# Performance work log

Hardware: AMD Instinct MI355X
Metric: run time of the kernel (lower is better)

## Reference

```python
import jax, jax.numpy as jnp
import numpy as np

N, K, C, R, S = 10000, 16, 32, 32, 64
D = 9  # per-channel irrep dim of interaction feats: 0e(1)+1o(3)+2e(5)
AVG_NEIGH = 16.0
EPS = 1e-6

_rng = np.random.default_rng(0)
# fixed constant coupling tensors (deterministic stand-ins for CG coefficients; structure matches e3nn paths)
CG112 = jnp.asarray(_rng.standard_normal((3, 3, 5)) * 0.2, jnp.float32)  # 1o x 1o -> 2e
CG121 = jnp.asarray(_rng.standard_normal((3, 5, 3)) * 0.2, jnp.float32)  # 1o x 2e -> 1o
# symmetric tensor-product bases U[order, ir_out]: shape (D,)*order + (mul, ir_dim)
MULS = {3: {'0e': 3, '1o': 2}, 2: {'0e': 2, '1o': 1}, 1: {'0e': 1, '1o': 1}}
IRDIM = {'0e': 1, '1o': 3}
U = {(o, ir): jnp.asarray(_rng.standard_normal((D,) * o + (MULS[o][ir], IRDIM[ir])) * (0.3 ** o), jnp.float32)
     for o in (3, 2, 1) for ir in ('0e', '1o')}


def _normnorm(arrs):
    # E3NormNorm: per-node RMS normalization over channel/component axes
    return [a / jnp.sqrt(jnp.mean(a * a, axis=tuple(range(1, a.ndim)), keepdims=True) + EPS) for a in arrs]


def _sph_harm(vec):
    # real spherical harmonics l=1,2 (component normalization) on normalized vectors
    r = vec / (jnp.linalg.norm(vec, axis=-1, keepdims=True) + EPS)
    x, y, z = r[..., 0], r[..., 1], r[..., 2]
    sh1 = jnp.sqrt(3.0) * r
    c = jnp.sqrt(15.0)
    sh2 = jnp.stack([c * x * y, c * y * z, jnp.sqrt(5.0) / 2 * (3 * z * z - 1), c * x * z, c / 2 * (x * x - y * y)], axis=-1)
    return sh1, sh2


def _forward(node_s, node_v, vectors, radial_embedding, species_table, Wu0, Wu1, radW, radb, ln_g, ln_b,
             Wd0, Wd1, Wd2, w3_0e, w3_1o, w2_0e, w2_1o, w1_0e, w1_1o, P0, P1, Wskip0, Wskip1, Wread,
             receivers, node_specie):
    n, c = node_s.shape
    inv = 1.0 / jnp.sqrt(1.0 * c)
    # ---- InteractionBlock: linear_up + norm ----
    s = node_s @ Wu0 * inv
    v = jnp.einsum('nci,cd->ndi', node_v, Wu1) * inv
    s, v = _normnorm([s, v])
    # ---- MessagePassingConvolution: sender = node i broadcast over its K=16 neighbors ----
    sh1, sh2 = _sph_harm(vectors)  # [n,K,3], [n,K,5]
    m0a = jnp.broadcast_to(s[:, None, :], (n, K, c))                       # prefix 0e
    m0b = jnp.einsum('nci,nki->nkc', v, sh1) / jnp.sqrt(3.0)               # 1o x 1o -> 0e
    m1a = jnp.broadcast_to(v[:, None], (n, K, c, 3))                       # prefix 1o
    m1b = jnp.einsum('nc,nki->nkci', s, sh1) / jnp.sqrt(3.0)               # 0e x 1o -> 1o
    m1c = jnp.einsum('nci,nkp,ipj->nkcj', v, sh2, CG121)                   # 1o x 2e -> 1o
    m2a = jnp.einsum('nc,nkp->nkcp', s, sh2) / jnp.sqrt(5.0)               # 0e x 2e -> 2e
    m2b = jnp.einsum('nci,nkj,ijp->nkcp', v, sh1, CG112)                   # 1o x 1o -> 2e
    M0 = jnp.concatenate([m0a, m0b], axis=-1)      # [n,K,2C]
    M1 = jnp.concatenate([m1a, m1b, m1c], axis=2)  # [n,K,3C,3]
    M2 = jnp.concatenate([m2a, m2b], axis=2)       # [n,K,2C,5]
    # radial mix: linear + layernorm, one weight per irrep (7C total)
    rad = radial_embedding @ radW + radb
    mu = rad.mean(-1, keepdims=True)
    var = rad.var(-1, keepdims=True)
    rad = ln_g * (rad - mu) / jnp.sqrt(var + EPS) + ln_b
    r0, r1, r2 = rad[..., :2 * c], rad[..., 2 * c:5 * c], rad[..., 5 * c:]
    M0 = M0 * r0
    M1 = M1 * r1[..., None]
    M2 = M2 * r2[..., None]
    # scatter-add messages to receivers, normalize by sqrt(avg_num_neighbors)
    idx = receivers.reshape(-1)
    sc = 1.0 / jnp.sqrt(AVG_NEIGH)
    o0 = jnp.zeros((n, 2 * c), M0.dtype).at[idx].add(M0.reshape(n * K, 2 * c)) * sc
    o1 = jnp.zeros((n, 3 * c, 3), M1.dtype).at[idx].add(M1.reshape(n * K, 3 * c, 3)) * sc
    o2 = jnp.zeros((n, 2 * c, 5), M2.dtype).at[idx].add(M2.reshape(n * K, 2 * c, 5)) * sc
    o0, o1, o2 = _normnorm([o0, o1, o2])
    # linear_down to interaction_irreps Cx(0e+1o+2e), then norm
    A0 = o0 @ Wd0 / jnp.sqrt(2.0 * c)
    A1 = jnp.einsum('nmi,md->ndi', o1, Wd1) / jnp.sqrt(3.0 * c)
    A2 = jnp.einsum('nmi,md->ndi', o2, Wd2) / jnp.sqrt(2.0 * c)
    A0, A1, A2 = _normnorm([A0, A1, A2])
    # ---- EquivariantProductBasisBlock: species-gathered symmetric contraction ----
    x_sym = jnp.concatenate([A0[:, :, None], A1, A2], axis=-1)  # [n, C, D=9]
    species_ind = species_table[node_specie]                    # [n, R]
    Wsym = {(3, '0e'): w3_0e, (3, '1o'): w3_1o, (2, '0e'): w2_0e, (2, '1o'): w2_1o, (1, '0e'): w1_0e, (1, '1o'): w1_1o}
    out = {}
    for order in (3, 2, 1):
        for ir in ('0e', '1o'):
            u = U[(order, ir)]
            w = jnp.einsum('be,ekc->bkc', species_ind, Wsym[(order, ir)])
            if ir not in out:
                out[ir] = ('new', jnp.einsum('...jki,bkc,bcj->bc...i', u, w, x_sym))
            else:
                out[ir] = out[ir] + jnp.einsum('...ki,bkc->bc...i', u, w)
        for ir in ('0e', '1o'):
            if isinstance(out[ir], tuple):
                out[ir] = out[ir][1]  # creation order already consumed one x
            else:
                out[ir] = jnp.einsum('bc...ji,bcj->bc...i', out[ir], x_sym)
    sym_s = out['0e'][..., 0]  # [n, C]
    sym_v = out['1o']          # [n, C, 3]
    # proj_out linear
    ps = sym_s @ P0 * inv
    pv = jnp.einsum('nci,cd->ndi', sym_v, P1) * inv
    # species-indexed skip connection
    skip_s = jnp.einsum('nc,ncd->nd', node_s, Wskip0[node_specie]) * inv
    skip_v = jnp.einsum('nci,ncd->ndi', node_v, Wskip1[node_specie]) * inv
    s_out = ps + skip_s
    v_out = pv + skip_v
    # linear readout (output_irreps = 1x0e)
    read = s_out @ Wread * inv
    return jnp.concatenate([s_out, v_out.reshape(n, 3 * c), read], axis=-1)


def setup_inputs():
    ks = jax.random.split(jax.random.key(0), 32)
    f = lambda i, shape: jax.random.normal(ks[i], shape, jnp.float32)
    return {
        'node_s': f(0, (N, C)),
        'node_v': f(1, (N, C, 3)),
        'vectors': f(2, (N, K, 3)),
        'radial_embedding': f(3, (N, K, R)),
        'receivers': jax.random.randint(ks[4], (N, K), 0, N),
        'node_specie': jax.random.randint(ks[5], (N,), 0, S),
        'species_table': f(6, (S, R)),
        'Wu0': f(7, (C, C)), 'Wu1': f(8, (C, C)),
        'radW': f(9, (R, 7 * C)), 'radb': jnp.zeros((7 * C,), jnp.float32),
        'ln_g': jnp.ones((7 * C,), jnp.float32), 'ln_b': jnp.zeros((7 * C,), jnp.float32),
        'Wd0': f(11, (2 * C, C)), 'Wd1': f(12, (3 * C, C)), 'Wd2': f(13, (2 * C, C)),
        'w3_0e': f(14, (R, 3, C)), 'w3_1o': f(15, (R, 2, C)),
        'w2_0e': f(16, (R, 2, C)), 'w2_1o': f(17, (R, 1, C)),
        'w1_0e': f(18, (R, 1, C)), 'w1_1o': f(19, (R, 1, C)),
        'P0': f(20, (C, C)), 'P1': f(21, (C, C)),
        'Wskip0': f(22, (S, C, C)), 'Wskip1': f(23, (S, C, C)),
        'Wread': f(24, (C, 1)),
    }


def reference(node_s, node_v, vectors, radial_embedding, receivers, node_specie, species_table, Wu0, Wu1,
              radW, radb, ln_g, ln_b, Wd0, Wd1, Wd2, w3_0e, w3_1o, w2_0e, w2_1o, w1_0e, w1_1o,
              P0, P1, Wskip0, Wskip1, Wread):
    return _forward(node_s, node_v, vectors, radial_embedding, species_table, Wu0, Wu1, radW, radb, ln_g, ln_b,
                    Wd0, Wd1, Wd2, w3_0e, w3_1o, w2_0e, w2_1o, w1_0e, w1_1o, P0, P1, Wskip0, Wskip1, Wread,
                    receivers, node_specie)
```

## Files before the change

### kernel.cpp

```cpp
#include <hip/hip_runtime.h>
#include <cmath>
#include <stdint.h>

typedef unsigned long long u64;
typedef unsigned __int128 u128;

#define EPSF 1e-6f

#define OFF_RAW 0L
#define OFF_S   7168L
#define OFF_G   8960L
#define GSP_SZ  28032L
#define OFF_SN  (OFF_G + 64L*GSP_SZ)
#define OFF_VN  (OFF_SN + 320000L)
#define FLOAT_END (OFF_VN + 960000L)
#define OFF_RAD (FLOAT_END + 262144L)
#define RAD_REQ_BYTES ((size_t)(OFF_RAD + 35840000L) * 4)

#define IOFF_DEG   0
#define IOFF_OFFS  10000
#define IOFF_CUR   20001
#define IOFF_EL    30001
#define IOFF_SCNT  190001
#define IOFF_SOFF  190065
#define IOFF_SCUR  190130
#define IOFF_NORD  190194
#define IOFF_TRI   200194
#define IOFF_PAIR  200359


__device__ __forceinline__ u128 pcg_mul128() {
  return ((u128)2549297995355413924ULL << 64) | (u128)4865540595714422341ULL;
}
struct Pcg {
  u128 state, inc;
  __device__ __forceinline__ u64 next() {
    state = state * pcg_mul128() + inc;
    u64 hi = (u64)(state >> 64), lo = (u64)state;
    unsigned rot = (unsigned)(hi >> 58);
    u64 x = hi ^ lo;
    return (x >> rot) | (x << ((64u - rot) & 63u));
  }
};
__device__ __forceinline__ double u64_to_dbl(u64 u) {
  return (double)(u >> 11) * (1.0 / 9007199254740992.0);
}
__device__ __forceinline__ unsigned ss_hashmix(unsigned v, unsigned &hc) {
  v ^= hc; hc *= 0x931e8875u; v *= hc; v ^= v >> 16; return v;
}
__device__ __forceinline__ unsigned ss_mix(unsigned x, unsigned y) {
  unsigned r = 0xca01f9ddu * x - 0x4973f715u * y; r ^= r >> 16; return r;
}

#define NBUF 8192
#define NBM  8191
#define PERTH 32
#define NDRAW 7092
#define NSEG  222

__global__ __launch_bounds__(256) void k_constants(float* __restrict__ wsf, int* __restrict__ wsi)
{
  __shared__ double wi[256], fi[256];
  __shared__ u64 ki[256];
  __shared__ u64 buf[NBUF];
  __shared__ float zv[NBUF];
  __shared__ unsigned char cons[NBUF];
  __shared__ unsigned short jmp[NBUF];
  __shared__ unsigned short heads[NSEG];
  __shared__ u64 sseed[4];
  __shared__ u64 stst[512], enst[512];
  __shared__ double scl[8];
  __shared__ int flag;
  const int tid = threadIdx.x;
  float* raw = wsf + OFF_RAW;

  if (tid == 0) {
    flag = 0;
    unsigned hc = 0x43b0d7e5u;
    unsigned pool[4];
    for (int i = 0; i < 4; i++) pool[i] = ss_hashmix(0u, hc);
    for (int s = 0; s < 4; s++)
      for (int d = 0; d < 4; d++)
        if (s != d) pool[d] = ss_mix(pool[d], ss_hashmix(pool[s], hc));
    unsigned hb = 0x8b51f9ddu;
    u64 sw[4];
    {
      unsigned w8[8];
      for (int i = 0; i < 8; i++) {
        unsigned dv = pool[i & 3];
        dv ^= hb; hb *= 0x58f38dedu; dv *= hb; dv ^= dv >> 16;
        w8[i] = dv;
      }
      for (int k2 = 0; k2 < 4; k2++) sw[k2] = (u64)w8[2*k2] | ((u64)w8[2*k2+1] << 32);
    }
    u128 initstate = ((u128)sw[0] << 64) | (u128)sw[1];
    u128 initseq   = ((u128)sw[2] << 64) | (u128)sw[3];
    u128 inc_ = (initseq << 1) | (u128)1;
    u128 S0 = inc_;
    S0 += initstate;
    S0 = S0 * pcg_mul128() + inc_;
    sseed[0] = (u64)(S0 >> 64);   sseed[1] = (u64)S0;
    sseed[2] = (u64)(inc_ >> 64); sseed[3] = (u64)inc_;
    double p2 = pow(0.3, 2.0), p3 = pow(0.3, 3.0);
    scl[0]=0.2; scl[1]=0.2; scl[2]=p3; scl[3]=p3; scl[4]=p2; scl[5]=p2; scl[6]=0.3; scl[7]=0.3;
    const double m1 = 4503599627370496.0;
    const double ZR = 3.6541528853610087963519472518;
    double dn = ZR, tn = ZR;
    const double vn = 4.92867323399e-3;
    double fv = exp(-0.5 * dn * dn);
    double q = vn / fv;
    ki[0] = (u64)((dn / q) * m1);
    ki[1] = 0;
    wi[0] = q / m1;  wi[255] = dn / m1;
    fi[0] = 1.0;     fi[255] = fv;
    for (int i = 254; i >= 1; i--) {
      dn = sqrt(-2.0 * log(vn / dn + fv));
      ki[i+1] = (u64)((dn / tn) * m1);
      tn = dn;
      fv = exp(-0.5 * dn * dn);
      fi[i] = fv;
      wi[i] = dn / m1;
    }
    int mcnt = 0;
    for (int a = 0; a < 9; a++)
      for (int b = a; b < 9; b++)
        for (int j3 = b; j3 < 9; j3++)
          wsi[IOFF_TRI + (mcnt++)] = a | (b << 4) | (j3 << 8);
    int pcnt = 0;
    for (int a = 0; a < 9; a++)
      for (int b = a; b < 9; b++)
        wsi[IOFF_PAIR + (pcnt++)] = a | (b << 4);
  }
  __syncthreads();

  {
    u128 S0   = ((u128)sseed[0] << 64) | (u128)sseed[1];
    u128 inc_ = ((u128)sseed[2] << 64) | (u128)sseed[3];
    u128 aR = (u128)1, cR = (u128)0;
    u128 aP = pcg_mul128(), cP = inc_;
    unsigned e = (unsigned)tid * PERTH;
    while (e) {
      if (e & 1u) { cR = aP * cR + cP; aR = aP * aR; }
      cP = aP * cP + cP;
      aP = aP * aP;
      e >>= 1;
    }
    Pcg g; g.inc = inc_; g.state = aR * S0 + cR;
    stst[tid*2] = (u64)(g.state >> 64); stst[tid*2+1] = (u64)g.state;
    #pragma unroll 4
    for (int k = 0; k < PERTH; k++) buf[tid*PERTH + k] = g.next();
    enst[tid*2] = (u64)(g.state >> 64); enst[tid*2+1] = (u64)g.state;
  }
  __syncthreads();
  if (tid < 255) {
    if (stst[(tid+1)*2] != enst[tid*2] || stst[(tid+1)*2+1] != enst[tid*2+1])
      atomicOr(&flag, 1);
  }
  if (tid == 0) {
    if (fabs(u64_to_dbl(buf[0]) - 0.6369616873214543) > 1e-12) atomicOr(&flag, 1);
  }
  __syncthreads();
  if (flag && tid == 0) {
    u128 S0   = ((u128)sseed[0] << 64) | (u128)sseed[1];
    u128 inc_ = ((u128)sseed[2] << 64) | (u128)sseed[3];
    Pcg g; g.state = S0; g.inc = inc_;
    for (int k = 0; k < NBUF; k++) buf[k] = g.next();
  }
  __syncthreads();

  const double ZRd  = 3.6541528853610087963519472518;
  const double ZIRd = 0.27366123732975827203338247596;
  for (int k = 0; k < PERTH; k++) {
    const int p = tid*PERTH + k;
    int pos = p;
    int consumed = 0;
    double z = 0.0;
    u64 r = buf[pos & NBM]; pos++; consumed++;
    for (int guard = 0; guard < 64; guard++) {
      int idx = (int)(r & 0xff);
      r >>= 8;
      int sgn = (int)(r & 1);
      u64 rabs = (r >> 1) & 0x000fffffffffffffULL;
      double x = (double)rabs * wi[idx];
      if (sgn) x = -x;
      if (rabs < ki[idx]) { z = x; break; }
      if (idx == 0) {
        double xx = 0.0, yy = 0.0;
        for (int g2 = 0; g2 < 64; g2++) {
          u64 ua = buf[pos & NBM]; pos++; consumed++;
          u64 ub = buf[pos & NBM]; pos++; consumed++;
          xx = -ZIRd * log1p(-u64_to_dbl(ua));
          yy = -log1p(-u64_to_dbl(ub));
          if (yy + yy > xx * xx) break;
        }
        z = ((rabs >> 8) & 1) ? -(ZRd + xx) : (ZRd + xx);
        break;
      } else {
        u64 u = buf[pos & NBM]; pos++; consumed++;
        if ((fi[idx-1] - fi[idx]) * u64_to_dbl(u) + fi[idx] < exp(-0.5 * x * x)) { z = x; break; }
      }
      r = buf[pos & NBM]; pos++; consumed++;
    }
    zv[p] = (float)z;
    cons[p] = (unsigned char)(consumed > 255 ? 255 : consumed);
  }
  __syncthreads();

  {
    int pos[PERTH];
    #pragma unroll
    for (int k = 0; k < PERTH; k++) pos[k] = tid*PERTH + k;
    for (int s = 0; s < 32; s++) {
      #pragma unroll
      for (int k = 0; k < PERTH; k++) {
        int np = pos[k] + (int)cons[pos[k]];
        pos[k] = (np > NBM) ? NBM : np;
      }
    }
    #pragma unroll
    for (int k = 0; k < PERTH; k++) jmp[tid*PERTH + k] = (unsigned short)pos[k];
  }
  __syncthreads();

  if (tid == 0) {
    int pos = 0;
    for (int m = 0; m < NSEG; m++) { heads[m] = (unsigned short)pos; pos = (int)jmp[pos]; }
  }
  __syncthreads();

  if (tid < NSEG) {
    int pos = (int)heads[tid];
    const int i0 = tid * 32;
    for (int k = 0; k < 32; k++) {
      const int i = i0 + k;
      if (i >= NDRAW) break;
      double sc;
      if      (i < 90)   sc = scl[0];
      else if (i < 6651) sc = scl[2];
      else if (i < 7056) sc = scl[4];
      else               sc = scl[6];
      raw[i] = (float)((double)zv[pos] * sc);
      int np = pos + (int)cons[pos];
      pos = (np > NBM) ? NBM : np;
    }
  }
}

__global__ __launch_bounds__(256) void k_stables(float* __restrict__ wsf, const int* __restrict__ wsi)
{
  const int tid = threadIdx.x;
  const float* raw = wsf + OFF_RAW;
  float* Sb = wsf + OFF_S;
  for (int idx = tid; idx < 495; idx += 256) {
    int m = idx / 3, k2 = idx % 3;
    int tp = wsi[IOFF_TRI + m];
    int a = tp & 15, b = (tp >> 4) & 15, j3 = (tp >> 8) & 15;
    int P[6][3] = {{a,b,j3},{a,j3,b},{b,a,j3},{b,j3,a},{j3,a,b},{j3,b,a}};
    float s = 0.f;
    for (int t = 0; t < 6; t++) {
      bool dup = false;
      for (int u = 0; u < t; u++)
        if (P[u][0]==P[t][0] && P[u][1]==P[t][1] && P[u][2]==P[t][2]) { dup = true; break; }
      if (!dup) s += raw[90 + ((P[t][0]*9 + P[t][1])*9 + P[t][2])*3 + k2];
    }
    Sb[m*3 + k2] = s;
  }
  for (int idx = tid; idx < 990; idx += 256) {
    int m = idx / 6, r6 = idx % 6, k2 = r6 / 3, i = r6 % 3;
    int tp = wsi[IOFF_TRI + m];
    int a = tp & 15, b = (tp >> 4) & 15, j3 = (tp >> 8) & 15;
    int P[6][3] = {{a,b,j3},{a,j3,b},{b,a,j3},{b,j3,a},{j3,a,b},{j3,b,a}};
    float s = 0.f;
    for (int t = 0; t < 6; t++) {
      bool dup = false;
      for (int u = 0; u < t; u++)
        if (P[u][0]==P[t][0] && P[u][1]==P[t][1] && P[u][2]==P[t][2]) { dup = true; break; }
      if (!dup) s += raw[2277 + (((P[t][0]*9 + P[t][1])*9 + P[t][2])*2 + k2)*3 + i];
    }
    Sb[495 + (m*2 + k2)*3 + i] = s;
  }
  for (int idx = tid; idx < 90; idx += 256) {
    int m = idx / 2, k2 = idx % 2;
    int pp = wsi[IOFF_PAIR + m]; int a = pp & 15, b = (pp >> 4) & 15;
    float s = raw[6651 + (a*9 + b)*2 + k2];
    if (a != b) s += raw[6651 + (b*9 + a)*2 + k2];
    Sb[1485 + idx] = s;
  }
  for (int idx = tid; idx < 135; idx += 256) {
    int m = idx / 3, i = idx % 3;
    int pp = wsi[IOFF_PAIR + m]; int a = pp & 15, b = (pp >> 4) & 15;
    float s = raw[6813 + (a*9 + b)*3 + i];
    if (a != b) s += raw[6813 + (b*9 + a)*3 + i];
    Sb[1575 + idx] = s;
  }
  for (int idx = tid; idx < 9;  idx += 256) Sb[1710 + idx] = raw[7056 + idx];
  for (int idx = tid; idx < 27; idx += 256) Sb[1719 + idx] = raw[7065 + idx];
}

__global__ __launch_bounds__(256) void k_gtable(
    const float* __restrict__ stab,
    const float* __restrict__ w30e, const float* __restrict__ w31o,
    const float* __restrict__ w20e, const float* __restrict__ w21o,
    const float* __restrict__ w10e, const float* __restrict__ w11o,
    float* __restrict__ wsf)
{
  const int sp = blockIdx.x, tid = threadIdx.x;
  float* Gsp = wsf + OFF_G + (long)sp * GSP_SZ;
  __shared__ float st[32];
  if (tid < 32) st[tid] = stab[sp*32 + tid];
  __syncthreads();
  for (int t = tid; t < 320; t += 256) {
    const float* W; int kc, kcs;
    if (t < 96)       { W = w30e; kc = t;       kcs = 96; }
    else if (t < 160) { W = w31o; kc = t - 96;  kcs = 64; }
    else if (t < 224) { W = w20e; kc = t - 160; kcs = 64; }
    else if (t < 256) { W = w21o; kc = t - 224; kcs = 32; }
    else if (t < 288) { W = w10e; kc = t - 256; kcs = 32; }
    else              { W = w11o; kc = t - 288; kcs = 32; }
    float a = 0.f;
    for (int e = 0; e < 32; e++) a += st[e] * W[e*kcs + kc];
    Gsp[t] = a;
  }
}

__global__ __launch_bounds__(256) void k_nodeupd(
    const float* __restrict__ ns, const float* __restrict__ nv,
    const float* __restrict__ Wu0, const float* __restrict__ Wu1,
    float* __restrict__ wsf)
{
  const int tid = threadIdx.x;
  const int nn = blockIdx.x * 8 + (tid >> 5);
  const int c = tid & 31;
  const float INV = 0.17677669529663687f;
  float s = 0.f;
  for (int e = 0; e < 32; e++) s += ns[nn*32 + e] * Wu0[e*32 + c];
  s *= INV;
  float v0 = 0, v1 = 0, v2 = 0;
  for (int e = 0; e < 32; e++) {
    const float w = Wu1[e*32 + c];
    const float* p = nv + (long)(nn*32 + e)*3;
    v0 += p[0]*w; v1 += p[1]*w; v2 += p[2]*w;
  }
  v0 *= INV; v1 *= INV; v2 *= INV;
  float ss = s*s;
  for (int m = 16; m >= 1; m >>= 1) ss += __shfl_xor(ss, m);
  float sv = v0*v0 + v1*v1 + v2*v2;
  for (int m = 16; m >= 1; m >>= 1) sv += __shfl_xor(sv, m);
  float rs = rsqrtf(ss * (1.f/32.f) + EPSF);
  float rv = rsqrtf(sv * (1.f/96.f) + EPSF);
  wsf[OFF_SN + nn*32 + c] = s * rs;
  float* vp = wsf + OFF_VN + (long)(nn*32 + c)*3;
  vp[0] = v0*rv; vp[1] = v1*rv; vp[2] = v2*rv;
}

#define RB_E 32
__global__ __launch_bounds__(256) void k_radial(
    const float* __restrict__ remb, const float* __restrict__ radW,
    const float* __restrict__ radb, const float* __restrict__ ln_g,
    const float* __restrict__ ln_b, float* __restrict__ wsf)
{
  __shared__ float er[RB_E][33];
  __shared__ __align__(16) float pre[RB_E][224];
  __shared__ float4 lg4[56], lb4[56];
  const int tid = threadIdx.x;
  const long e0 = (long)blockIdx.x * RB_E;

  if (tid < 56) { lg4[tid] = ((const float4*)ln_g)[tid]; lb4[tid] = ((const float4*)ln_b)[tid]; }
  for (int i = tid; i < RB_E*32; i += 256) {
    const int e = i >> 5, q = i & 31;
    er[e][q] = remb[(e0 + e)*32 + q];
  }
  __syncthreads();

  if (tid < 224) {
    const int cg = tid % 56, grp = tid / 56;
    const float4 rb = ((const float4*)radb)[cg];
    float4 acc[8];
    #pragma unroll
    for (int k = 0; k < 8; k++) acc[k] = rb;
    const float4* radW4 = (const float4*)radW;
    for (int q = 0; q < 32; q++) {
      const float4 w = radW4[q*56 + cg];
      #pragma unroll
      for (int k = 0; k < 8; k++) {
        const float ev = er[grp*8 + k][q];
        acc[k].x = fmaf(ev, w.x, acc[k].x);
        acc[k].y = fmaf(ev, w.y, acc[k].y);
        acc[k].z = fmaf(ev, w.z, acc[k].z);
        acc[k].w = fmaf(ev, w.w, acc[k].w);
      }
    }
    #pragma unroll
    for (int k = 0; k < 8; k++)
      ((float4*)&pre[grp*8 + k][0])[cg] = acc[k];
  }
  __syncthreads();

  const int wv = tid >> 6, ln = tid & 63;
  for (int k = 0; k < 8; k++) {
    const int e = wv*8 + k;
    float a0 = 0.f, a1 = 0.f, a2 = 0.f, a3 = 0.f;
    if (ln < 56) {
      const float4 v = ((const float4*)&pre[e][0])[ln];
      a0 = v.x; a1 = v.y; a2 = v.z; a3 = v.w;
    }
    float c1 = a0 + a1 + a2 + a3;
    float c2 = a0*a0 + a1*a1 + a2*a2 + a3*a3;
    for (int m = 32; m >= 1; m >>= 1) { c1 += __shfl_xor(c1, m); c2 += __shfl_xor(c2, m); }
    const float mu = c1 * (1.f/224.f);
    const float rvar = rsqrtf(c2*(1.f/224.f) - mu*mu + EPSF);
    if (ln < 56) {
      const float4 lg = lg4[ln], lb = lb4[ln];
      float4 o;
      o.x = lg.x*(a0-mu)*rvar + lb.x;
      o.y = lg.y*(a1-mu)*rvar + lb.y;
      o.z = lg.z*(a2-mu)*rvar + lb.z;
      o.w = lg.w*(a3-mu)*rvar + lb.w;
      ((float4*)(wsf + OFF_RAD))[(e0 + e)*56 + ln] = o;
    }
  }
}

__global__ void k_zero(int* __restrict__ wsi) {
  int i = blockIdx.x*256 + threadIdx.x;
  if (i < 10000) { wsi[IOFF_DEG + i] = 0; wsi[IOFF_CUR + i] = 0; }
  if (i < 64)    { wsi[IOFF_SCNT + i] = 0; wsi[IOFF_SCUR + i] = 0; }
}
__global__ void k_hist(const int* __restrict__ recv, const int* __restrict__ spec, int* __restrict__ wsi) {
  int e = blockIdx.x*256 + threadIdx.x;
  if (e < 160000) atomicAdd(&wsi[IOFF_DEG + recv[e]], 1);
  if (e < 10000)  atomicAdd(&wsi[IOFF_SCNT + spec[e]], 1);
}
__global__ __launch_bounds__(1024) void k_scan(int* __restrict__ wsi) {
  __shared__ int part[1024];
  const int tid = threadIdx.x;
  int loc[10];
  int base = tid * 10;
  int s = 0;
  for (int t = 0; t < 10; t++) {
    int idx = base + t;
    loc[t] = s;
    s += (idx < 10000) ? wsi[IOFF_DEG + idx] : 0;
  }
  part[tid] = s;
  __syncthreads();
  for (int d = 1; d < 1024; d <<= 1) {
    int v = (tid >= d) ? part[tid - d] : 0;
    __syncthreads();
    part[tid] += v;
    __syncthreads();
  }
  int exc = (tid > 0) ? part[tid - 1] : 0;
  for (int t = 0; t < 10; t++) {
    int idx = base + t;
    if (idx <= 10000) wsi[IOFF_OFFS + idx] = exc + loc[t];
  }
  if (tid == 0) {
    int a = 0;
    for (int s2 = 0; s2 < 64; s2++) { wsi[IOFF_SOFF + s2] = a; a += wsi[IOFF_SCNT + s2]; }
    wsi[IOFF_SOFF + 64] = a;
  }
}
__global__ void k_fill(const int* __restrict__ recv, const int* __restrict__ spec, int* __restrict__ wsi) {
  int e = blockIdx.x*256 + threadIdx.x;
  if (e < 160000) {
    int r = recv[e];
    int p = atomicAdd(&wsi[IOFF_CUR + r], 1);
    wsi[IOFF_EL + wsi[IOFF_OFFS + r] + p] = e;
  }
  if (e < 10000) {
    int sp = spec[e];
    int p = atomicAdd(&wsi[IOFF_SCUR + sp], 1);
    wsi[IOFF_NORD + wsi[IOFF_SOFF + sp] + p] = e;
  }
}

__device__ __forceinline__ float msg_fast(int slot,
    const float* __restrict__ se, const float* __restrict__ ve,
    const float* __restrict__ sh, const float* __restrict__ ab,
    const float* __restrict__ rd)
{
  const float IS3 = 0.57735026918962576f;
  const float IS5 = 0.44721359549995794f;
  float val; int radidx;
  if (slot < 64) {
    radidx = slot;
    if (slot < 32) val = se[slot];
    else {
      int c = slot - 32;
      val = (ve[c*3+0]*sh[0] + ve[c*3+1]*sh[1] + ve[c*3+2]*sh[2]) * IS3;
    }
  } else if (slot < 352) {
    int q = slot - 64; int row = q / 3; int i = q - row*3;
    radidx = 64 + row;
    if (row < 32) val = ve[row*3 + i];
    else if (row < 64) val = se[row - 32] * sh[i] * IS3;
    else {
      int c = row - 64;
      val = ve[c*3+0]*ab[0+i] + ve[c*3+1]*ab[3+i] + ve[c*3+2]*ab[6+i];
    }
  } else {
    int q = slot - 352; int row = q / 5; int p = q - row*5;
    radidx = 160 + row;
    if (row < 32) val = se[row] * sh[3+p] * IS5;
    else {
      int c = row - 32;
      val = ve[c*3+0]*ab[9+p] + ve[c*3+1]*ab[14+p] + ve[c*3+2]*ab[19+p];
    }
  }
  return val * rd[radidx];
}

#define SM_RAD 0
#define SM_SE  896
#define SM_VE  1024
#define SM_ER  1408
#define SM_SHH 1536
#define SM_AB  1568
#define SM_LNG 1664
#define SM_LNB 1888
#define SM_RB  2112
#define SM_CG  2336
#define SM_S    0
#define SM_X    1746
#define SM_O    2034
#define SM_GRED 2706
#define SM_SYMS 3730
#define SM_SYMV 3762
#define SM_SOUT 3858
#define SM_REDB 3890
#define SM_RF   3902
#define SMEM_N  3906

template<int PRE>
__global__ __launch_bounds__(256) void k_main(
    const float* __restrict__ node_s, const float* __restrict__ node_v,
    const float* __restrict__ vectors, const float* __restrict__ remb,
    const int* __restrict__ nspec,
    const float* __restrict__ radW, const float* __restrict__ radb,
    const float* __restrict__ ln_g, const float* __restrict__ ln_b,
    const float* __restrict__ Wd0, const float* __restrict__ Wd1, const float* __restrict__ Wd2,
    const float* __restrict__ P0, const float* __restrict__ P1,
    const float* __restrict__ Wsk0, const float* __restrict__ Wsk1,
    const float* __restrict__ Wread,
    const float* __restrict__ wsf, const int* __restrict__ wsi,
    float* __restrict__ out)
{
  const int tid = threadIdx.x;
  const int wv  = tid >> 6;
  const int ln  = tid & 63;
  __shared__ __align__(16) float smem[SMEM_N];
  __shared__ int tri_s[165], pair_s[45];

  const int j  = wsi[IOFF_NORD + blockIdx.x];
  const int sp = nspec[j];
  const int e0 = wsi[IOFF_OFFS + j];
  const int e1 = wsi[IOFF_OFFS + j + 1];

  if (!PRE) {
    for (int i = tid; i < 224; i += 256) {
      smem[SM_LNG + i] = ln_g[i];
      smem[SM_LNB + i] = ln_b[i];
      smem[SM_RB  + i] = radb[i];
    }
  }
  for (int i = tid; i < 90; i += 256) smem[SM_CG + i] = wsf[OFF_RAW + i];
  __syncthreads();

  float acc0 = 0.f, acc1 = 0.f, acc2 = 0.f;
  for (int t = e0; t < e1; t += 4) {
    const int eidx = t + wv;
    const bool act = (eidx < e1);
    if (act) {
      const int e = wsi[IOFF_EL + eidx];
      const int n = e >> 4;
      if (ln < 32) {
        smem[SM_SE + wv*32 + ln] = wsf[OFF_SN + (long)n*32 + ln];
        if (!PRE) smem[SM_ER + wv*32 + ln] = remb[(long)e*32 + ln];
      } else {
        const int l2 = ln - 32;
        const float* vp = wsf + OFF_VN + (long)(n*32 + l2)*3;
        smem[SM_VE + wv*96 + l2*3+0] = vp[0];
        smem[SM_VE + wv*96 + l2*3+1] = vp[1];
        smem[SM_VE + wv*96 + l2*3+2] = vp[2];
      }
      if (ln == 0) {
        const float* vv = vectors + (long)e*3;
        float vx = vv[0], vy = vv[1], vz = vv[2];
        float nr = sqrtf(vx*vx + vy*vy + vz*vz) + EPSF;
        float rx = vx/nr, ry = vy/nr, rz = vz/nr;
        smem[SM_SHH + wv*8 + 0] = 1.7320508075688772f * rx;
        smem[SM_SHH + wv*8 + 1] = 1.7320508075688772f * ry;
        smem[SM_SHH + wv*8 + 2] = 1.7320508075688772f * rz;
        smem[SM_SHH + wv*8 + 3] = 3.872983346207417f * rx*ry;
        smem[SM_SHH + wv*8 + 4] = 3.872983346207417f * ry*rz;
        smem[SM_SHH + wv*8 + 5] = 1.118033988749895f * (3.f*rz*rz - 1.f);
        smem[SM_SHH + wv*8 + 6] = 3.872983346207417f * rx*rz;
        smem[SM_SHH + wv*8 + 7] = 1.9364916731037085f * (rx*rx - ry*ry);
      }
      if (PRE) {
        if (ln < 56) {
          const float4 v4 = ((const float4*)(wsf + OFF_RAD))[(long)e*56 + ln];
          ((float4*)&smem[SM_RAD + wv*224])[ln] = v4;
        }
      } else {
        float aval[4];
        float c1 = 0.f, c2 = 0.f;
        #pragma unroll
        for (int k = 0; k < 4; k++) {
          const int ch = ln + 64*k;
          if (ch < 224) {
            float a = smem[SM_RB + ch];
            #pragma unroll 8
            for (int q = 0; q < 32; q++)
              a += smem[SM_ER + wv*32 + q] * radW[q*224 + ch];
            aval[k] = a; c1 += a; c2 += a*a;
          }
        }
        for (int m = 32; m >= 1; m >>= 1) { c1 += __shfl_xor(c1, m); c2 += __shfl_xor(c2, m); }
        const float mu = c1 * (1.f/224.f);
        const float rvar = rsqrtf(c2*(1.f/224.f) - mu*mu + EPSF);
        #pragma unroll
        for (int k = 0; k < 4; k++) {
          const int ch = ln + 64*k;
          if (ch < 224)
            smem[SM_RAD + wv*224 + ch] = smem[SM_LNG + ch]*(aval[k]-mu)*rvar + smem[SM_LNB + ch];
        }
      }
      if (ln < 9) {
        const int i2 = ln / 3, i = ln - i2*3;
        float a = 0.f;
        #pragma unroll
        for (int p = 0; p < 5; p++)
          a += smem[SM_SHH + wv*8 + 3 + p] * smem[SM_CG + 45 + i2*15 + p*3 + i];
        smem[SM_AB + wv*24 + ln] = a;
      } else if (ln < 24) {
        const int q = ln - 9, i = q / 5, p = q - i*5;
        float a = 0.f;
        #pragma unroll
        for (int j2 = 0; j2 < 3; j2++)
          a += smem[SM_SHH + wv*8 + j2] * smem[SM_CG + i*15 + j2*5 + p];
        smem[SM_AB + wv*24 + 9 + q] = a;
      }
    }
    __syncthreads();
    const int nact = (e1 - t < 4) ? (e1 - t) : 4;
    for (int w = 0; w < nact; w++) {
      const float* se = &smem[SM_SE + w*32];
      const float* ve = &smem[SM_VE + w*96];
      const float* sh = &smem[SM_SHH + w*8];
      const float* ab = &smem[SM_AB + w*24];
      const float* rd = &smem[SM_RAD + w*224];
      acc0 += msg_fast(tid,       se, ve, sh, ab, rd);
      acc1 += msg_fast(tid + 256, se, ve, sh, ab, rd);
      if (tid < 160) acc2 += msg_fast(tid + 512, se, ve, sh, ab, rd);
    }
    __syncthreads();
  }

  for (int i = tid; i < 1746; i += 256) smem[SM_S + i] = wsf[OFF_S + i];
  for (int i = tid; i < 165; i += 256) tri_s[i] = wsi[IOFF_TRI + i];
  for (int i = tid; i < 45;  i += 256) pair_s[i] = wsi[IOFF_PAIR + i];

  float* redbuf = &smem[SM_REDB];
  float* rf     = &smem[SM_RF];
  acc0 *= 0.25f; acc1 *= 0.25f; acc2 *= 0.25f;
  float g0 = 0, g1 = 0, g2 = 0;
  if (tid < 64) g0 = acc0*acc0; else g1 = acc0*acc0;
  if (tid < 96) g1 += acc1*acc1; else g2 += acc1*acc1;
  if (tid < 160) g2 += acc2*acc2;
  for (int m = 32; m >= 1; m >>= 1) { g0 += __shfl_xor(g0, m); g1 += __shfl_xor(g1, m); g2 += __shfl_xor(g2, m); }
  if ((tid & 63) == 0) { redbuf[wv] = g0; redbuf[4+wv] = g1; redbuf[8+wv] = g2; }
  __syncthreads();
  if (tid == 0) {
    float s0 = redbuf[0]+redbuf[1]+redbuf[2]+redbuf[3];
    float s1 = redbuf[4]+redbuf[5]+redbuf[6]+redbuf[7];
    float s2 = redbuf[8]+redbuf[9]+redbuf[10]+redbuf[11];
    rf[0] = rsqrtf(s0*(1.f/64.f)  + EPSF);
    rf[1] = rsqrtf(s1*(1.f/288.f) + EPSF);
    rf[2] = rsqrtf(s2*(1.f/320.f) + EPSF);
  }
  __syncthreads();
  smem[SM_O + tid]       = acc0 * ((tid < 64) ? rf[0] : rf[1]);
  smem[SM_O + tid + 256] = acc1 * ((tid < 96) ? rf[1] : rf[2]);
  if (tid < 160) smem[SM_O + tid + 512] = acc2 * rf[2];
  __syncthreads();

  const float* o_lds = &smem[SM_O];
  float av1, av2 = 0.f;
  if (tid < 32) {
    float a = 0;
    for (int m = 0; m < 64; m++) a += o_lds[m] * Wd0[m*32 + tid];
    av1 = a * 0.125f;
  } else if (tid < 128) {
    int q = tid - 32, d = q/3, i = q - d*3;
    float a = 0;
    for (int m = 0; m < 96; m++) a += o_lds[64 + m*3 + i] * Wd1[m*32 + d];
    av1 = a * 0.10206207261596575f;
  } else {
    int q = tid - 128, d = q/5, p = q - d*5;
    float a = 0;
    for (int m = 0; m < 64; m++) a += o_lds[352 + m*5 + p] * Wd2[m*32 + d];
    av1 = a * 0.125f;
  }
  if (tid < 32) {
    int q = tid + 128, d = q/5, p = q - d*5;
    float a = 0;
    for (int m = 0; m < 64; m++) a += o_lds[352 + m*5 + p] * Wd2[m*32 + d];
    av2 = a * 0.125f;
  }
  float p0 = (tid < 32) ? av1*av1 : 0.f;
  float p1 = (tid >= 32 && tid < 128) ? av1*av1 : 0.f;
  float p2s = (tid >= 128) ? av1*av1 : 0.f;
  if (tid < 32) p2s += av2*av2;
  for (int m = 32; m >= 1; m >>= 1) { p0 += __shfl_xor(p0, m); p1 += __shfl_xor(p1, m); p2s += __shfl_xor(p2s, m); }
  if ((tid & 63) == 0) { redbuf[wv] = p0; redbuf[4+wv] = p1; redbuf[8+wv] = p2s; }
  __syncthreads();
  if (tid == 0) {
    float s0 = redbuf[0]+redbuf[1]+redbuf[2]+redbuf[3];
    float s1 = redbuf[4]+redbuf[5]+redbuf[6]+redbuf[7];
    float s2 = redbuf[8]+redbuf[9]+redbuf[10]+redbuf[11];
    rf[0] = rsqrtf(s0*(1.f/32.f)  + EPSF);
    rf[1] = rsqrtf(s1*(1.f/96.f)  + EPSF);
    rf[2] = rsqrtf(s2*(1.f/160.f) + EPSF);
  }
  __syncthreads();
  float* x_lds = &smem[SM_X];
  if (tid < 32) x_lds[tid*9 + 0] = av1 * rf[0];
  else if (tid < 128) { int q = tid - 32, d = q/3, i = q - d*3; x_lds[d*9 + 1 + i] = av1 * rf[1]; }
  else { int q = tid - 128, d = q/5, p = q - d*5; x_lds[d*9 + 4 + p] = av1 * rf[2]; }
  if (tid < 32) { int q = tid + 128, d = q/5, p = q - d*5; x_lds[d*9 + 4 + p] = av2 * rf[2]; }
  __syncthreads();

  const float* Sb = &smem[SM_S];
  float* gred = &smem[SM_GRED];
  const int c = tid & 31, g = tid >> 5;
  float xr[9];
  for (int t2 = 0; t2 < 9; t2++) xr[t2] = x_lds[c*9 + t2];
  const float* wl = wsf + OFF_G + (long)sp * GSP_SZ;
  const float w30a = wl[c], w30b = wl[32 + c], w30c = wl[64 + c];
  const float w31a = wl[96 + c], w31b = wl[128 + c];
  const float w20a = wl[160 + c], w20b = wl[192 + c];
  const float w21  = wl[224 + c];
  const float w10  = wl[256 + c];
  const float w11  = wl[288 + c];

  float sa = 0, va0 = 0, va1 = 0, va2 = 0;
  for (int m = g; m < 165; m += 8) {
    const int tp = tri_s[m];
    const float P = xr[tp & 15] * xr[(tp >> 4) & 15] * xr[(tp >> 8) & 15];
    sa += P * (Sb[m*3+0]*w30a + Sb[m*3+1]*w30b + Sb[m*3+2]*w30c);
    const float* s1p = &Sb[495 + m*6];
    va0 += P * (s1p[0]*w31a + s1p[3]*w31b);
    va1 += P * (s1p[1]*w31a + s1p[4]*w31b);
    va2 += P * (s1p[2]*w31a + s1p[5]*w31b);
  }
  for (int m = g; m < 45; m += 8) {
    const int pp = pair_s[m];
    const float P = xr[pp & 15] * xr[(pp >> 4) & 15];
    sa += P * (Sb[1485 + m*2+0]*w20a + Sb[1485 + m*2+1]*w20b);
    const float* s1p = &Sb[1575 + m*3];
    va0 += P * s1p[0] * w21;
    va1 += P * s1p[1] * w21;
    va2 += P * s1p[2] * w21;
  }
  if (g == 0) {
    for (int a = 0; a < 9; a++) {
      const float xa = xr[a];
      sa += xa * Sb[1710 + a] * w10;
      va0 += xa * Sb[1719 + a*3 + 0] * w11;
      va1 += xa * Sb[1719 + a*3 + 1] * w11;
      va2 += xa * Sb[1719 + a*3 + 2] * w11;
    }
  }
  gred[0*256 + g*32 + c] = sa;
  gred[1*256 + g*32 + c] = va0;
  gred[2*256 + g*32 + c] = va1;
  gred[3*256 + g*32 + c] = va2;
  __syncthreads();
  float* syms = &smem[SM_SYMS];
  float* symv = &smem[SM_SYMV];
  float* sout = &smem[SM_SOUT];
  if (tid < 128) {
    int cc = tid & 31, comp = tid >> 5;
    float a = 0;
    for (int gg = 0; gg < 8; gg++) a += gred[comp*256 + gg*32 + cc];
    if (comp == 0) syms[cc] = a; else symv[cc*3 + comp - 1] = a;
  }
  __syncthreads();

  const float INV = 0.17677669529663687f;
  if (tid < 32) {
    int d = tid; float ps = 0, sk = 0;
    const float* Wp = Wsk0 + (long)sp * 1024;
    for (int c2 = 0; c2 < 32; c2++) {
      ps += syms[c2] * P0[c2*32 + d];
      sk += node_s[j*32 + c2] * Wp[c2*32 + d];
    }
    float val = (ps + sk) * INV;
    sout[d] = val;
    out[(long)j*129 + d] = val;
  } else if (tid < 128) {
    int q = tid - 32, d = q/3, i = q - d*3;
    float pv = 0, sk = 0;
    const float* Wp = Wsk1 + (long)sp * 1024;
    for (int c2 = 0; c2 < 32; c2++) {
      pv += symv[c2*3 + i] * P1[c2*32 + d];
      sk += node_v[(long)(j*32 + c2)*3 + i] * Wp[c2*32 + d];
    }
    out[(long)j*129 + 32 + q] = (pv + sk) * INV;
  }
  __syncthreads();
  if (tid < 32) {
    float p = sout[tid] * Wread[tid];
    for (int m = 16; m >= 1; m >>= 1) p += __shfl_xor(p, m);
    if (tid == 0) out[(long)j*129 + 128] = p * INV;
  }
}

extern "C" void kernel_launch(void* const* d_in, const int* in_sizes, int n_in,
                              void* d_out, int out_size, void* d_ws, size_t ws_size,
                              hipStream_t stream)
{
  const float* node_s  = (const float*)d_in[0];
  const float* node_v  = (const float*)d_in[1];
  const float* vectors = (const float*)d_in[2];
  const float* remb    = (const float*)d_in[3];
  const int*   recv    = (const int*)d_in[4];
  const int*   nspec   = (const int*)d_in[5];
  const float* stab    = (const float*)d_in[6];
  const float* Wu0     = (const float*)d_in[7];
  const float* Wu1     = (const float*)d_in[8];
  const float* radW    = (const float*)d_in[9];
  const float* radb    = (const float*)d_in[10];
  const float* ln_g    = (const float*)d_in[11];
  const float* ln_b    = (const float*)d_in[12];
  const float* Wd0     = (const float*)d_in[13];
  const float* Wd1     = (const float*)d_in[14];
  const float* Wd2     = (const float*)d_in[15];
  const float* w30e    = (const float*)d_in[16];
  const float* w31o    = (const float*)d_in[17];
  const float* w20e    = (const float*)d_in[18];
  const float* w21o    = (const float*)d_in[19];
  const float* w10e    = (const float*)d_in[20];
  const float* w11o    = (const float*)d_in[21];
  const float* P0      = (const float*)d_in[22];
  const float* P1      = (const float*)d_in[23];
  const float* Wsk0    = (const float*)d_in[24];
  const float* Wsk1    = (const float*)d_in[25];
  const float* Wread   = (const float*)d_in[26];
  float* out = (float*)d_out;
  float* wsf = (float*)d_ws;
  int*   wsi = (int*)((char*)d_ws + FLOAT_END * sizeof(float));

  const bool pre = (ws_size >= RAD_REQ_BYTES);

  k_constants<<<1, 256, 0, stream>>>(wsf, wsi);
  k_stables<<<1, 256, 0, stream>>>(wsf, wsi);
  k_zero<<<40, 256, 0, stream>>>(wsi);
  k_nodeupd<<<1250, 256, 0, stream>>>(node_s, node_v, Wu0, Wu1, wsf);
  if (pre) k_radial<<<5000, 256, 0, stream>>>(remb, radW, radb, ln_g, ln_b, wsf);
  k_hist<<<625, 256, 0, stream>>>(recv, nspec, wsi);
  k_scan<<<1, 1024, 0, stream>>>(wsi);
  k_fill<<<625, 256, 0, stream>>>(recv, nspec, wsi);
  k_gtable<<<64, 256, 0, stream>>>(stab, w30e, w31o, w20e, w21o, w10e, w11o, wsf);
  if (pre) {
    k_main<1><<<10000, 256, 0, stream>>>(node_s, node_v, vectors, remb, nspec,
                                         radW, radb, ln_g, ln_b, Wd0, Wd1, Wd2,
                                         P0, P1, Wsk0, Wsk1, Wread, wsf, wsi, out);
  } else {
    k_main<0><<<10000, 256, 0, stream>>>(node_s, node_v, vectors, remb, nspec,
                                         radW, radb, ln_g, ln_b, Wd0, Wd1, Wd2,
                                         P0, P1, Wsk0, Wsk1, Wread, wsf, wsi, out);
  }
}
```

Measured before the change: 654.8 us.

## Precompute per-species fused symmetric-contraction tables and merge stable kernel into constants

The symmetric-basis tables are now multiplied with the per-species weights ahead of time in k_gtable, giving a full per-species table (about 28K floats) that the main kernel reads directly from global memory. This removes the per-block copy of the 1746-float basis into shared memory and the per-term weight multiplies in the contraction loop. The stables computation is folded into k_constants, saving one launch, and the tri/pair index loads move before the edge loop. In exchange each block reads a larger species table from global/L2, and k_gtable does more work.

```diff
diff --git a/kernel.cpp b/kernel.cpp
--- a/kernel.cpp
+++ b/kernel.cpp
@@ -244,12 +244,8 @@
       pos = (np > NBM) ? NBM : np;
     }
   }
-}
-
-__global__ __launch_bounds__(256) void k_stables(float* __restrict__ wsf, const int* __restrict__ wsi)
-{
-  const int tid = threadIdx.x;
-  const float* raw = wsf + OFF_RAW;
+  __syncthreads();
+
   float* Sb = wsf + OFF_S;
   for (int idx = tid; idx < 495; idx += 256) {
     int m = idx / 3, k2 = idx % 3;
@@ -305,8 +301,10 @@
     float* __restrict__ wsf)
 {
   const int sp = blockIdx.x, tid = threadIdx.x;
+  const float* Sb = wsf + OFF_S;
   float* Gsp = wsf + OFF_G + (long)sp * GSP_SZ;
   __shared__ float st[32];
+  __shared__ float wl[320];
   if (tid < 32) st[tid] = stab[sp*32 + tid];
   __syncthreads();
   for (int t = tid; t < 320; t += 256) {
@@ -319,7 +317,38 @@
     else              { W = w11o; kc = t - 288; kcs = 32; }
     float a = 0.f;
     for (int e = 0; e < 32; e++) a += st[e] * W[e*kcs + kc];
-    Gsp[t] = a;
+    wl[t] = a;
+  }
+  __syncthreads();
+  for (int idx = tid; idx < 5280; idx += 256) {
+    int m = idx >> 5, c = idx & 31;
+    float a = 0;
+    for (int k = 0; k < 3; k++) a += Sb[m*3 + k] * wl[k*32 + c];
+    Gsp[idx] = a;
+  }
+  for (int idx = tid; idx < 15840; idx += 256) {
+    int m = idx / 96, r = idx % 96, i = r >> 5, c = r & 31;
+    float a = 0;
+    for (int k = 0; k < 2; k++) a += Sb[495 + (m*2 + k)*3 + i] * wl[96 + k*32 + c];
+    Gsp[5280 + idx] = a;
+  }
+  for (int idx = tid; idx < 1440; idx += 256) {
+    int m = idx >> 5, c = idx & 31;
+    float a = 0;
+    for (int k = 0; k < 2; k++) a += Sb[1485 + m*2 + k] * wl[160 + k*32 + c];
+    Gsp[21120 + idx] = a;
+  }
+  for (int idx = tid; idx < 4320; idx += 256) {
+    int m = idx / 96, r = idx % 96, i = r >> 5, c = r & 31;
+    Gsp[22560 + idx] = Sb[1575 + m*3 + i] * wl[224 + c];
+  }
+  for (int idx = tid; idx < 288; idx += 256) {
+    int a2 = idx >> 5, c = idx & 31;
+    Gsp[26880 + idx] = Sb[1710 + a2] * wl[256 + c];
+  }
+  for (int idx = tid; idx < 864; idx += 256) {
+    int a2 = idx / 96, r = idx % 96, i = r >> 5, c = r & 31;
+    Gsp[27168 + idx] = Sb[1719 + a2*3 + i] * wl[288 + c];
   }
 }
 
@@ -521,13 +550,12 @@
 #define SM_LNB 1888
 #define SM_RB  2112
 #define SM_CG  2336
-#define SM_S    0
-#define SM_X    1746
-#define SM_O    2034
-#define SM_GRED 2706
-#define SM_SYMS 3730
-#define SM_SYMV 3762
-#define SM_SOUT 3858
+#define SM_X    0
+#define SM_O    288
+#define SM_GRED 960
+#define SM_SYMS 1984
+#define SM_SYMV 2016
+#define SM_SOUT 2112
 #define SM_REDB 3890
 #define SM_RF   3902
 #define SMEM_N  3906
@@ -565,6 +593,8 @@
     }
   }
   for (int i = tid; i < 90; i += 256) smem[SM_CG + i] = wsf[OFF_RAW + i];
+  for (int i = tid; i < 165; i += 256) tri_s[i] = wsi[IOFF_TRI + i];
+  for (int i = tid; i < 45;  i += 256) pair_s[i] = wsi[IOFF_PAIR + i];
   __syncthreads();
 
   float acc0 = 0.f, acc1 = 0.f, acc2 = 0.f;
@@ -658,10 +688,6 @@
     __syncthreads();
   }
 
-  for (int i = tid; i < 1746; i += 256) smem[SM_S + i] = wsf[OFF_S + i];
-  for (int i = tid; i < 165; i += 256) tri_s[i] = wsi[IOFF_TRI + i];
-  for (int i = tid; i < 45;  i += 256) pair_s[i] = wsi[IOFF_PAIR + i];
-
   float* redbuf = &smem[SM_REDB];
   float* rf     = &smem[SM_RF];
   acc0 *= 0.25f; acc1 *= 0.25f; acc2 *= 0.25f;
@@ -732,45 +758,33 @@
   if (tid < 32) { int q = tid + 128, d = q/5, p = q - d*5; x_lds[d*9 + 4 + p] = av2 * rf[2]; }
   __syncthreads();
 
-  const float* Sb = &smem[SM_S];
   float* gred = &smem[SM_GRED];
   const int c = tid & 31, g = tid >> 5;
   float xr[9];
   for (int t2 = 0; t2 < 9; t2++) xr[t2] = x_lds[c*9 + t2];
-  const float* wl = wsf + OFF_G + (long)sp * GSP_SZ;
-  const float w30a = wl[c], w30b = wl[32 + c], w30c = wl[64 + c];
-  const float w31a = wl[96 + c], w31b = wl[128 + c];
-  const float w20a = wl[160 + c], w20b = wl[192 + c];
-  const float w21  = wl[224 + c];
-  const float w10  = wl[256 + c];
-  const float w11  = wl[288 + c];
+  const float* Gsp = wsf + OFF_G + (long)sp * GSP_SZ;
 
   float sa = 0, va0 = 0, va1 = 0, va2 = 0;
   for (int m = g; m < 165; m += 8) {
     const int tp = tri_s[m];
     const float P = xr[tp & 15] * xr[(tp >> 4) & 15] * xr[(tp >> 8) & 15];
-    sa += P * (Sb[m*3+0]*w30a + Sb[m*3+1]*w30b + Sb[m*3+2]*w30c);
-    const float* s1p = &Sb[495 + m*6];
-    va0 += P * (s1p[0]*w31a + s1p[3]*w31b);
-    va1 += P * (s1p[1]*w31a + s1p[4]*w31b);
-    va2 += P * (s1p[2]*w31a + s1p[5]*w31b);
+    sa += P * Gsp[m*32 + c];
+    const float* g3 = Gsp + 5280 + m*96 + c;
+    va0 += P*g3[0]; va1 += P*g3[32]; va2 += P*g3[64];
   }
   for (int m = g; m < 45; m += 8) {
     const int pp = pair_s[m];
     const float P = xr[pp & 15] * xr[(pp >> 4) & 15];
-    sa += P * (Sb[1485 + m*2+0]*w20a + Sb[1485 + m*2+1]*w20b);
-    const float* s1p = &Sb[1575 + m*3];
-    va0 += P * s1p[0] * w21;
-    va1 += P * s1p[1] * w21;
-    va2 += P * s1p[2] * w21;
+    sa += P * Gsp[21120 + m*32 + c];
+    const float* g2p = Gsp + 22560 + m*96 + c;
+    va0 += P*g2p[0]; va1 += P*g2p[32]; va2 += P*g2p[64];
   }
   if (g == 0) {
     for (int a = 0; a < 9; a++) {
-      const float xa = xr[a];
-      sa += xa * Sb[1710 + a] * w10;
-      va0 += xa * Sb[1719 + a*3 + 0] * w11;
-      va1 += xa * Sb[1719 + a*3 + 1] * w11;
-      va2 += xa * Sb[1719 + a*3 + 2] * w11;
+      const float P = xr[a];
+      sa += P * Gsp[26880 + a*32 + c];
+      const float* g1p = Gsp + 27168 + a*96 + c;
+      va0 += P*g1p[0]; va1 += P*g1p[32]; va2 += P*g1p[64];
     }
   }
   gred[0*256 + g*32 + c] = sa;
@@ -856,7 +870,6 @@
   const bool pre = (ws_size >= RAD_REQ_BYTES);
 
   k_constants<<<1, 256, 0, stream>>>(wsf, wsi);
-  k_stables<<<1, 256, 0, stream>>>(wsf, wsi);
   k_zero<<<40, 256, 0, stream>>>(wsi);
   k_nodeupd<<<1250, 256, 0, stream>>>(node_s, node_v, Wu0, Wu1, wsf);
   if (pre) k_radial<<<5000, 256, 0, stream>>>(remb, radW, radb, ln_g, ln_b, wsf);
```

Measured after the change: 676.0 us. +3.2%, slower.
